# Kernel tuning notes

Measured on AMD Instinct MI355X. Metric: run time of the kernel, lower is better.

## Reference

```python
import jax, jax.numpy as jnp
import numpy as np
from jax import lax

STRIDE = 1
PADDING = 1


def setup_inputs() -> dict:
    key = jax.random.key(0)
    kx, kw = jax.random.split(key)
    x = jax.random.normal(kx, (32, 64, 64, 64), dtype=jnp.float32)
    # weights are angles uniform on (-pi, pi)
    weight = jax.random.uniform(kw, (128, 64, 3, 3), dtype=jnp.float32,
                                minval=-jnp.pi, maxval=jnp.pi)
    return {"x": x, "weight": weight}


def _ring_conv2d(x, weight, stride, padding):
    # out[b,o,i,j] = sum_{c,kh,kw} cos(x_pad[b,c,i*s+kh,j*s+kw] - w[o,c,kh,kw])
    # cos(a-b) = cos a cos b + sin a sin b  ->  two standard convolutions.
    # Pad the raw angles with zeros first (a padded zero contributes cos(-w)).
    p = padding
    xp = jnp.pad(x, ((0, 0), (0, 0), (p, p), (p, p)))
    dn = ('NCHW', 'OIHW', 'NCHW')
    out = lax.conv_general_dilated(jnp.cos(xp), jnp.cos(weight),
                                   window_strides=(stride, stride),
                                   padding='VALID', dimension_numbers=dn)
    out = out + lax.conv_general_dilated(jnp.sin(xp), jnp.sin(weight),
                                         window_strides=(stride, stride),
                                         padding='VALID', dimension_numbers=dn)
    return out


def reference(x, weight):
    return _ring_conv2d(x, weight, STRIDE, PADDING)
```

## Files before the change

### kernel.cpp

```cpp
#include <hip/hip_runtime.h>
#include <hip/hip_bf16.h>


typedef _Float16 half8 __attribute__((ext_vector_type(8)));
typedef float f32x16 __attribute__((ext_vector_type(16)));

#define NB 32
#define NC 64
#define NH 64
#define NW 64
#define NO 128
#define PW 66
#define PSTRIDE 72
#define TROWS 10
#define TCOLS 34
#define TPX (TROWS * TCOLS)
#define NELEM (TPX * 16)
#define NPASS 22

union U16 { unsigned short u; _Float16 h; };
union HB { uint4 u4; unsigned long long q[2]; half8 h; };

__device__ inline unsigned pack_cs(float ang) {
    float s, c;
    sincosf(ang, &s, &c);
    U16 uc, us; uc.h = (_Float16)c; us.h = (_Float16)s;
    return (unsigned)uc.u | ((unsigned)us.u << 16);
}

__device__ inline unsigned pack_cs_fast(float ang) {
    float s, c;
    __sincosf(ang, &s, &c);
    U16 uc, us; uc.h = (_Float16)c; us.h = (_Float16)s;
    return (unsigned)uc.u | ((unsigned)us.u << 16);
}

__global__ __launch_bounds__(256) void prep_w(const float* __restrict__ w,
                                              uint4* __restrict__ wqa) {
    int tt = blockIdx.x * 256 + threadIdx.x;
    if (tt >= 36 * 2 * 128 * 2) return;
    int g2 = tt & 1, o = (tt >> 1) & 127, kk = (tt >> 8) & 1, chunk = tt >> 9;
    int cg = chunk / 9, kpos = chunk % 9, kh = kpos / 3, kw = kpos % 3;
    unsigned r[4];
#pragma unroll
    for (int m = 0; m < 4; ++m) {
        int c = cg * 16 + kk * 8 + g2 * 4 + m;
        float ang = w[((o * NC + c) * 3 + kh) * 3 + kw];
        r[m] = pack_cs(ang);
    }
    wqa[tt] = make_uint4(r[0], r[1], r[2], r[3]);
}

__global__ __launch_bounds__(256, 2) void ring_conv(const float* __restrict__ xr,
                                                    const uint4* __restrict__ wqa,
                                                    float* __restrict__ out) {
    __shared__ __align__(16) char xs[TPX * PSTRIDE];

    const int d = blockIdx.x;
    const int blk = (d & 7) * 64 + (d >> 3);

    const int ch2 = blk & 1, rq = (blk >> 1) & 7, b = blk >> 4;
    const int row0 = rq * 8, col0 = ch2 * 32;

    const int t = threadIdx.x, lane = t & 63, wid = t >> 6;
    const int l31 = lane & 31, g2 = lane >> 5;
    const int op = wid & 1, rg = wid >> 1;
    const int rowbase = rg * 4;

    f32x16 acc[2][4] = {};

    const float* xb = xr + (size_t)b * NC * NH * NW;
    const int xlane = l31 * PSTRIDE + g2 * 16;
    const uint4* wbase = wqa + (op * 64 + l31) * 2 + g2;

    unsigned vmask = 0;
#pragma unroll
    for (int k = 0; k < NPASS; ++k) {
        int e = k * 256 + t; if (e > NELEM - 1) e = NELEM - 1;
        int p = e % TPX;
        int rr = p / TCOLS, cc = p - rr * TCOLS;
        int gr = row0 - 1 + rr, gc = col0 - 1 + cc;
        if (((unsigned)gr < 64u) && ((unsigned)gc < 64u)) vmask |= 1u << k;
    }

    float S[NPASS];
    unsigned pk[NPASS];

#define STAGE_LOAD(cgi)                                                        \
    {   const float* src = xb + (size_t)(cgi) * 16 * NH * NW;                  \
        _Pragma("unroll")                                                      \
        for (int k = 0; k < NPASS; ++k) {                                      \
            int e = k * 256 + t; if (e > NELEM - 1) e = NELEM - 1;             \
            int c16 = e / TPX, p = e - c16 * TPX;                              \
            int rr = p / TCOLS, cc = p - rr * TCOLS;                           \
            int gr = row0 - 1 + rr, gc = col0 - 1 + cc;                        \
            gr = min(max(gr, 0), 63); gc = min(max(gc, 0), 63);                \
            S[k] = src[(c16 * NH + gr) * NW + gc];                             \
        } }

#define STAGE_PACK()                                                           \
    {   _Pragma("unroll")                                                      \
        for (int k = 0; k < NPASS; ++k) {                                      \
            float v = ((vmask >> k) & 1u) ? S[k] : 0.f;                        \
            pk[k] = pack_cs_fast(v);                                           \
        } }

#define STAGE_WRITE()                                                          \
    {   _Pragma("unroll")                                                      \
        for (int k = 0; k < NPASS; ++k) {                                      \
            int e = k * 256 + t; if (e > NELEM - 1) e = NELEM - 1;             \
            int c16 = e / TPX, p = e - c16 * TPX;                              \
            *(unsigned*)&xs[p * PSTRIDE + c16 * 4] = pk[k];                    \
        } }

    STAGE_LOAD(0)
    STAGE_PACK()
    STAGE_WRITE()
    __syncthreads();

    for (int cg = 0; cg < 4; ++cg) {
        const uint4* wa = wbase + (size_t)(cg * 18) * 256;

        HB Ar[4][2];
#pragma unroll
        for (int i = 0; i < 4; ++i) {
            Ar[i][0].u4 = wa[i * 256];
            Ar[i][1].u4 = wa[i * 256 + 64];
        }
        HB Bop[2][4];
#pragma unroll
        for (int r = 0; r < 4; ++r) {
            const char* sp = xs + (rowbase + r) * TCOLS * PSTRIDE + xlane;
            Bop[0][r].q[0] = *(const unsigned long long*)sp;
            Bop[0][r].q[1] = *(const unsigned long long*)(sp + 8);
        }

        if (cg < 3) STAGE_LOAD(cg + 1)

#pragma unroll
        for (int s = 0; s < 18; ++s) {
            const int cp = s & 1, np = cp ^ 1;
            if (s < 17) {
                const int s1 = s + 1, kp1 = s1 >> 1, kk1 = s1 & 1;
                const int kh1 = kp1 / 3, kw1 = kp1 % 3;
#pragma unroll
                for (int r = 0; r < 4; ++r) {
                    const char* sp = xs
                        + (((rowbase + r + kh1) * TCOLS + kw1) * PSTRIDE + kk1 * 32) + xlane;
                    Bop[np][r].q[0] = *(const unsigned long long*)sp;
                    Bop[np][r].q[1] = *(const unsigned long long*)(sp + 8);
                }
            }
            __builtin_amdgcn_s_setprio(1);
#pragma unroll
            for (int r = 0; r < 4; ++r)
#pragma unroll
                for (int f = 0; f < 2; ++f)
                    acc[f][r] = __builtin_amdgcn_mfma_f32_32x32x16_f16(
                        Ar[s & 3][f].h, Bop[cp][r].h, acc[f][r], 0, 0, 0);
            __builtin_amdgcn_s_setprio(0);
            if (s < 14) {
                Ar[s & 3][0].u4 = wa[(s + 4) * 256];
                Ar[s & 3][1].u4 = wa[(s + 4) * 256 + 64];
            }
        }

        if (cg < 3) {
            STAGE_PACK()
            __syncthreads();
            STAGE_WRITE()
            __syncthreads();
        }
    }

#pragma unroll
    for (int f = 0; f < 2; ++f)
#pragma unroll
        for (int r = 0; r < 4; ++r) {
            const int orow = row0 + rowbase + r;
#pragma unroll
            for (int reg = 0; reg < 16; ++reg) {
                int o = op * 64 + f * 32 + (reg & 3) + 8 * (reg >> 2) + 4 * g2;
                out[(((size_t)b * NO + o) * NH + orow) * NW + col0 + l31] = acc[f][r][reg];
            }
        }
}

extern "C" void kernel_launch(void* const* d_in, const int* in_sizes, int n_in,
                              void* d_out, int out_size, void* d_ws, size_t ws_size,
                              hipStream_t stream) {
    const float* x = (const float*)d_in[0];
    const float* w = (const float*)d_in[1];

    uint4* wqp = (uint4*)d_ws;

    prep_w<<<72, 256, 0, stream>>>(w, wqp);
    ring_conv<<<512, 256, 0, stream>>>(x, wqp, (float*)d_out);
}
```

Measured before the change: 65.62 us.

## Vectorize input staging with float4 loads and double-buffer the LDS tile

Input staging now uses 16-byte float4 global loads covering 4 columns per slot (7 per thread instead of 22 scalar loads), and packs and writes only the in-tile columns. The LDS tile is double-buffered, so the next channel group is written into the alternate buffer and one barrier per iteration replaces two. This reduces load instruction count, register pressure for staged values, and barrier stalls, at the cost of doubled LDS use (about 49KB) and some redundant loaded columns at tile edges. Out-of-range pixels are written as the packed (cos,sin) of zero directly.

```diff
diff --git a/kernel.cpp b/kernel.cpp
--- a/kernel.cpp
+++ b/kernel.cpp
@@ -10,13 +10,10 @@
 #define NH 64
 #define NW 64
 #define NO 128
-#define PW 66
 #define PSTRIDE 72
 #define TROWS 10
 #define TCOLS 34
 #define TPX (TROWS * TCOLS)
-#define NELEM (TPX * 16)
-#define NPASS 22
 
 union U16 { unsigned short u; _Float16 h; };
 union HB { uint4 u4; unsigned long long q[2]; half8 h; };
@@ -51,10 +48,10 @@
     wqa[tt] = make_uint4(r[0], r[1], r[2], r[3]);
 }
 
-__global__ __launch_bounds__(256, 2) void ring_conv(const float* __restrict__ xr,
+__global__ __launch_bounds__(256, 2) void ring_conv(const float* __restrict__ xraw,
                                                     const uint4* __restrict__ wqa,
                                                     float* __restrict__ out) {
-    __shared__ __align__(16) char xs[TPX * PSTRIDE];
+    __shared__ __align__(16) char xs[2][TPX * PSTRIDE];
 
     const int d = blockIdx.x;
     const int blk = (d & 7) * 64 + (d >> 3);
@@ -69,57 +66,62 @@
 
     f32x16 acc[2][4] = {};
 
-    const float* xb = xr + (size_t)b * NC * NH * NW;
+    int roff[7];
+#pragma unroll
+    for (int k = 0; k < 7; ++k) {
+        int slot = k * 256 + t;
+        if (slot > 1599) slot = 1599;
+        int chn = slot / 100, rem = slot - chn * 100;
+        int row = rem / 10, cq = rem - row * 10;
+        int gr = row0 - 1 + row;
+        gr = min(max(gr, 0), 63);
+        int gc0 = col0 - 4 + cq * 4;
+        gc0 = min(max(gc0, 0), 60);
+        roff[k] = (chn * 64 + gr) * 64 + gc0;
+    }
+    const float* xb = xraw + (size_t)b * NC * NH * NW;
+
+#define PACKW(Sarr, dst)                                                        \
+    {   _Pragma("unroll")                                                       \
+        for (int k = 0; k < 7; ++k) {                                           \
+            int slot = k * 256 + t;                                             \
+            if (slot <= 1599) {                                                 \
+                int chn = slot / 100, rem = slot - chn * 100;                   \
+                int row = rem / 10, cq = rem - row * 10;                        \
+                int gr = row0 - 1 + row;                                        \
+                bool rok = ((unsigned)gr < 64u);                                \
+                int gc0 = col0 - 4 + cq * 4;                                    \
+                _Pragma("unroll")                                               \
+                for (int i = 0; i < 4; ++i) {                                   \
+                    int gc = gc0 + i;                                           \
+                    int cc = gc - col0 + 1;                                     \
+                    if ((unsigned)cc <= 33u) {                                  \
+                        bool ok = rok && ((unsigned)gc < 64u);                  \
+                        float vv = ((const float*)&Sarr[k])[i];                 \
+                        unsigned pk = ok ? pack_cs_fast(vv) : 0x00003C00u;      \
+                        int px = row * 34 + cc;                                 \
+                        *(unsigned*)&dst[px * PSTRIDE + (chn >> 2) * 16         \
+                                         + (chn & 3) * 4] = pk;                 \
+                    }                                                           \
+                }                                                               \
+            }                                                                   \
+        } }
+
     const int xlane = l31 * PSTRIDE + g2 * 16;
     const uint4* wbase = wqa + (op * 64 + l31) * 2 + g2;
 
-    unsigned vmask = 0;
-#pragma unroll
-    for (int k = 0; k < NPASS; ++k) {
-        int e = k * 256 + t; if (e > NELEM - 1) e = NELEM - 1;
-        int p = e % TPX;
-        int rr = p / TCOLS, cc = p - rr * TCOLS;
-        int gr = row0 - 1 + rr, gc = col0 - 1 + cc;
-        if (((unsigned)gr < 64u) && ((unsigned)gc < 64u)) vmask |= 1u << k;
-    }
-
-    float S[NPASS];
-    unsigned pk[NPASS];
-
-#define STAGE_LOAD(cgi)                                                        \
-    {   const float* src = xb + (size_t)(cgi) * 16 * NH * NW;                  \
-        _Pragma("unroll")                                                      \
-        for (int k = 0; k < NPASS; ++k) {                                      \
-            int e = k * 256 + t; if (e > NELEM - 1) e = NELEM - 1;             \
-            int c16 = e / TPX, p = e - c16 * TPX;                              \
-            int rr = p / TCOLS, cc = p - rr * TCOLS;                           \
-            int gr = row0 - 1 + rr, gc = col0 - 1 + cc;                        \
-            gr = min(max(gr, 0), 63); gc = min(max(gc, 0), 63);                \
-            S[k] = src[(c16 * NH + gr) * NW + gc];                             \
-        } }
-
-#define STAGE_PACK()                                                           \
-    {   _Pragma("unroll")                                                      \
-        for (int k = 0; k < NPASS; ++k) {                                      \
-            float v = ((vmask >> k) & 1u) ? S[k] : 0.f;                        \
-            pk[k] = pack_cs_fast(v);                                           \
-        } }
-
-#define STAGE_WRITE()                                                          \
-    {   _Pragma("unroll")                                                      \
-        for (int k = 0; k < NPASS; ++k) {                                      \
-            int e = k * 256 + t; if (e > NELEM - 1) e = NELEM - 1;             \
-            int c16 = e / TPX, p = e - c16 * TPX;                              \
-            *(unsigned*)&xs[p * PSTRIDE + c16 * 4] = pk[k];                    \
-        } }
-
-    STAGE_LOAD(0)
-    STAGE_PACK()
-    STAGE_WRITE()
+    {
+        uint4 S[7];
+#pragma unroll
+        for (int k = 0; k < 7; ++k) S[k] = *(const uint4*)(xb + roff[k]);
+        PACKW(S, xs[0])
+    }
     __syncthreads();
 
+    int cur = 0;
     for (int cg = 0; cg < 4; ++cg) {
         const uint4* wa = wbase + (size_t)(cg * 18) * 256;
+        const char* xbuf = xs[cur];
 
         HB Ar[4][2];
 #pragma unroll
@@ -130,12 +132,17 @@
         HB Bop[2][4];
 #pragma unroll
         for (int r = 0; r < 4; ++r) {
-            const char* sp = xs + (rowbase + r) * TCOLS * PSTRIDE + xlane;
+            const char* sp = xbuf + (rowbase + r) * TCOLS * PSTRIDE + xlane;
             Bop[0][r].q[0] = *(const unsigned long long*)sp;
             Bop[0][r].q[1] = *(const unsigned long long*)(sp + 8);
         }
 
-        if (cg < 3) STAGE_LOAD(cg + 1)
+        uint4 S[7];
+        if (cg < 3) {
+            const float* src = xb + (size_t)(cg + 1) * 16 * NH * NW;
+#pragma unroll
+            for (int k = 0; k < 7; ++k) S[k] = *(const uint4*)(src + roff[k]);
+        }
 
 #pragma unroll
         for (int s = 0; s < 18; ++s) {
@@ -145,7 +152,7 @@
                 const int kh1 = kp1 / 3, kw1 = kp1 % 3;
 #pragma unroll
                 for (int r = 0; r < 4; ++r) {
-                    const char* sp = xs
+                    const char* sp = xbuf
                         + (((rowbase + r + kh1) * TCOLS + kw1) * PSTRIDE + kk1 * 32) + xlane;
                     Bop[np][r].q[0] = *(const unsigned long long*)sp;
                     Bop[np][r].q[1] = *(const unsigned long long*)(sp + 8);
@@ -166,11 +173,11 @@
         }
 
         if (cg < 3) {
-            STAGE_PACK()
-            __syncthreads();
-            STAGE_WRITE()
-            __syncthreads();
-        }
+            char* dstb = xs[cur ^ 1];
+            PACKW(S, dstb)
+        }
+        __syncthreads();
+        cur ^= 1;
     }
 
 #pragma unroll
```

Result: slower. 71.88 us (+9.5%).
